# Optimization experiments

Hardware: AMD Instinct MI355X
Metric: run time of the kernel (lower is better)

Reference implementation:

```python
import jax, jax.numpy as jnp
import numpy as np
from jax import lax

B, C, H, W = 8, 48, 256, 256
HEADS = 8
FCT = 16  # self.factor
EPS = 1e-12  # torch F.normalize eps


def setup_inputs() -> dict:
    key = jax.random.key(0)
    k1, k2, k3, k4 = jax.random.split(key, 4)
    x = jax.random.normal(k1, (B, C, H, W), dtype=jnp.float32)
    # qkv 1x1 conv (bias=False): weight (3*dim, dim)
    w_qkv = jax.random.normal(k2, (3 * C, C), dtype=jnp.float32) * 0.05
    # depthwise 3x3 conv, groups = 3*dim: OIHW with I=1
    w_dw = jax.random.normal(k3, (3 * C, 1, 3, 3), dtype=jnp.float32) * 0.05
    # project_out 1x1 conv
    w_proj = jax.random.normal(k4, (C, C), dtype=jnp.float32) * 0.05
    temperature = jnp.ones((HEADS, 1, 1), dtype=jnp.float32)
    return {"x": x, "w_qkv": w_qkv, "w_dw": w_dw, "w_proj": w_proj,
            "temperature": temperature}


def _to_tokens(t):
    # pixel_unshuffle(factor=16) + rearrange
    # 'b (head c fy fx) h w -> b head (fx fy) (c h w)'
    b = t.shape[0]
    c = C // HEADS
    h, w = H // FCT, W // FCT
    # (b, head, c, h, fy, w, fx): pixel_unshuffle channel order is (C, fy, fx)
    t = t.reshape(b, HEADS, c, h, FCT, w, FCT)
    # -> (b, head, fx, fy, c, h, w)
    t = t.transpose(0, 1, 6, 4, 2, 3, 5)
    return t.reshape(b, HEADS, FCT * FCT, c * h * w)


def _from_tokens(t):
    # inverse rearrange + pixel_shuffle(factor=16)
    b = t.shape[0]
    c = C // HEADS
    h, w = H // FCT, W // FCT
    t = t.reshape(b, HEADS, FCT, FCT, c, h, w)  # (b, head, fx, fy, c, h, w)
    # -> (b, head, c, h, fy, w, fx) so final is (b, C, h*FCT, w*FCT)
    t = t.transpose(0, 1, 4, 5, 3, 6, 2)
    return t.reshape(b, C, H, W)


def _l2norm(t):
    n = jnp.sqrt(jnp.sum(t * t, axis=-1, keepdims=True))
    return t / jnp.maximum(n, EPS)


def reference(x, w_qkv, w_dw, w_proj, temperature):
    # H, W are multiples of factor=16 -> pad/unpad are no-ops
    qkv = jnp.einsum('bchw,oc->bohw', x, w_qkv)  # 1x1 conv
    qkv = lax.conv_general_dilated(
        qkv, w_dw, window_strides=(1, 1), padding='SAME',
        feature_group_count=3 * C,
        dimension_numbers=('NCHW', 'OIHW', 'NCHW'))  # depthwise 3x3
    q, k, v = jnp.split(qkv, 3, axis=1)
    q = _l2norm(_to_tokens(q))  # (b, head, 256, c*h*w)
    k = _l2norm(_to_tokens(k))
    v = _to_tokens(v)
    attn = jnp.einsum('bhnd,bhmd->bhnm', q, k) * temperature[None]
    e = jnp.exp(attn)
    attn = e / (jnp.sum(e, axis=-1, keepdims=True) + 1.0)  # softmax_1
    out = jnp.einsum('bhnm,bhmd->bhnd', attn, v)
    out = _from_tokens(out)
    return jnp.einsum('bchw,oc->bohw', out, w_proj)  # project_out
```

## Files before the change

kernel.cpp:

```cpp
#include <hip/hip_runtime.h>
#include <stdint.h>


#define DI __device__ __forceinline__
typedef __attribute__((ext_vector_type(8))) short short8;
typedef __attribute__((ext_vector_type(4))) float f32x4;
typedef __attribute__((ext_vector_type(4))) unsigned short us4;

DI unsigned short f2bf(float f){
  unsigned u = __float_as_uint(f);
  unsigned r = (u + 0x7FFFu + ((u >> 16) & 1u)) >> 16;
  return (unsigned short)r;
}
DI float bf2f(unsigned short h){ return __uint_as_float(((unsigned)h) << 16); }

__global__ __launch_bounds__(256) void k_qkv(const float* __restrict__ x,
                                             const float* __restrict__ wq,
                                             unsigned short* __restrict__ qkv)
{
  __shared__ unsigned short sm[19584];
  unsigned short* const lA = sm;
  unsigned short* const lB = sm + 10368;
  const int t = threadIdx.x;
  const int g0 = blockIdx.x << 7;
  const int b  = g0 >> 16;
  const int p0 = g0 & 65535;

  for (int i = t; i < 9792; i += 256) ((unsigned*)sm)[i] = 0u;
  __syncthreads();
  for (int j = t; j < 6912; j += 256){
    int m = j / 48, k = j - m * 48;
    lA[m * 72 + k] = f2bf(wq[j]);
  }
  for (int j = t; j < 384; j += 256){
    int cp = j >> 4, nc = j & 15;
    const float* xr = x + ((size_t)(b * 48 + 2 * cp)) * 65536 + p0 + nc * 8;
    float4 a0 = *(const float4*)xr;
    float4 a1 = *(const float4*)(xr + 4);
    float4 b0 = *(const float4*)(xr + 65536);
    float4 b1 = *(const float4*)(xr + 65536 + 4);
    float r0[8] = {a0.x,a0.y,a0.z,a0.w,a1.x,a1.y,a1.z,a1.w};
    float r1[8] = {b0.x,b0.y,b0.z,b0.w,b1.x,b1.y,b1.z,b1.w};
    unsigned* dst = (unsigned*)lB;
    int cx = (nc & 7) << 2;
    #pragma unroll
    for (int i = 0; i < 8; i++)
      dst[(nc * 8 + i) * 36 + (cp ^ cx)] =
        (unsigned)f2bf(r0[i]) | ((unsigned)f2bf(r1[i]) << 16);
  }
  __syncthreads();

  const int lane = t & 63, wv = t >> 6;
  const int m15 = lane & 15, quad = lane >> 4;
  const int nw = wv << 5;
  f32x4 acc[9][2];
  f32x4 z = {0.f,0.f,0.f,0.f};
  #pragma unroll
  for (int i = 0; i < 9; i++){ acc[i][0] = z; acc[i][1] = z; }

  #pragma unroll
  for (int ks = 0; ks < 2; ks++){
    short8 bfr[2];
    #pragma unroll
    for (int nt = 0; nt < 2; nt++){
      int row = nw + nt * 16 + m15;
      bfr[nt] = *(const short8*)(lB + row * 72 + (((4 * ks + quad) ^ ((row >> 3) & 7)) << 3));
    }
    #pragma unroll
    for (int mt = 0; mt < 9; mt++){
      short8 afr = *(const short8*)(lA + (mt * 16 + m15) * 72 + ks * 32 + quad * 8);
      acc[mt][0] = __builtin_amdgcn_mfma_f32_16x16x32_bf16(afr, bfr[0], acc[mt][0], 0, 0, 0);
      acc[mt][1] = __builtin_amdgcn_mfma_f32_16x16x32_bf16(afr, bfr[1], acc[mt][1], 0, 0, 0);
    }
  }
  __syncthreads();
  #pragma unroll
  for (int mt = 0; mt < 9; mt++)
    #pragma unroll
    for (int nt = 0; nt < 2; nt++)
      #pragma unroll
      for (int r = 0; r < 4; r++)
        sm[(mt * 16 + quad * 4 + r) * 136 + nw + nt * 16 + m15] = f2bf(acc[mt][nt][r]);
  __syncthreads();
  for (int j = t; j < 2304; j += 256){
    int o = j >> 4, oc = j & 15;
    *(uint4*)(qkv + ((size_t)(b * 144 + o)) * 65536 + p0 + oc * 8) =
      *(const uint4*)(sm + o * 136 + oc * 8);
  }
}

__global__ __launch_bounds__(256, 6) void k_dw(const unsigned short* __restrict__ qkv,
                                               const float* __restrict__ wd,
                                               unsigned short* __restrict__ tok0)
{
  __shared__ unsigned short tile[5184];
  __shared__ unsigned short lout[4224];
  const int t = threadIdx.x;
  const int wg = blockIdx.x, h = blockIdx.y;
  const int b = blockIdx.z / 72, g = blockIdx.z % 72;
  const int ch0 = g * 2;
  const int y0 = h << 4, xg = wg << 7;

  for (int j = t; j < 576; j += 256){
    int rowch = j >> 4, seg = j & 15;
    int cl = rowch >= 18, row = rowch - cl * 18;
    int y = y0 - 1 + row;
    uint4 v = {0u,0u,0u,0u};
    if ((unsigned)y < 256u)
      v = *(const uint4*)(qkv + ((size_t)(b*144 + ch0 + cl))*65536 + y*256 + xg + seg*8);
    *(uint4*)(tile + cl*2592 + row*144 + 8 + seg*8) = v;
  }
  if (t < 72){
    int rowch = t >> 1, side = t & 1;
    int cl = rowch >= 18, row = rowch - cl * 18;
    int y = y0 - 1 + row;
    int xx = side ? (xg + 128) : (xg - 1);
    unsigned short v = 0;
    if ((unsigned)y < 256u && (unsigned)xx < 256u)
      v = qkv[((size_t)(b*144 + ch0 + cl))*65536 + y*256 + xx];
    tile[cl*2592 + row*144 + (side ? 136 : 7)] = v;
  }
  __syncthreads();

  const int xt = t & 31, ys = t >> 5;
  const int x0 = xt << 2;
  #pragma unroll
  for (int cl = 0; cl < 2; cl++){
    int ch = ch0 + cl;
    float w9[9];
    #pragma unroll
    for (int i = 0; i < 9; i++) w9[i] = wd[ch * 9 + i];
    float f[4][6];
    #pragma unroll
    for (int rr = 0; rr < 4; rr++){
      const unsigned short* rp = tile + cl*2592 + (2*ys + rr)*144;
      us4 m = *(const us4*)(rp + 8 + x0);
      unsigned short a = rp[7 + x0];
      unsigned short bb = rp[12 + x0];
      f[rr][0] = bf2f(a);
      f[rr][1] = bf2f(m.x); f[rr][2] = bf2f(m.y);
      f[rr][3] = bf2f(m.z); f[rr][4] = bf2f(m.w);
      f[rr][5] = bf2f(bb);
    }
    #pragma unroll
    for (int r = 0; r < 2; r++)
      #pragma unroll
      for (int k = 0; k < 4; k++){
        float s = 0.f;
        #pragma unroll
        for (int dy = 0; dy < 3; dy++)
          #pragma unroll
          for (int dx = 0; dx < 3; dx++)
            s = fmaf(f[r + dy][k + dx], w9[dy * 3 + dx], s);
        int xl = x0 + k, yo = 2 * ys + r;
        int n = ((xl & 15) << 4) + yo;
        lout[cl*2112 + (xl >> 4)*264 + ((n & 0xF0) | ((n & 15) ^ (n >> 4)))] = f2bf(s);
      }
  }
  __syncthreads();
  for (int j = t; j < 512; j += 256){
    int cl = j >> 8, wt = (j >> 5) & 7, oc = j & 31;
    int split = ch0 / 48;
    int chs = ch0 - split * 48 + cl;
    int head = chs / 6, cc = chs - head * 6;
    int d = cc * 256 + h * 16 + wg * 8 + wt;
    const unsigned short* lp = lout + cl * 2112 + wt * 264;
    unsigned short v8[8];
    #pragma unroll
    for (int i = 0; i < 8; i++){
      int n = oc * 8 + i;
      v8[i] = lp[(n & 0xF0) | ((n & 15) ^ (n >> 4))];
    }
    uint4 pk;
    pk.x = (unsigned)v8[0] | ((unsigned)v8[1] << 16);
    pk.y = (unsigned)v8[2] | ((unsigned)v8[3] << 16);
    pk.z = (unsigned)v8[4] | ((unsigned)v8[5] << 16);
    pk.w = (unsigned)v8[6] | ((unsigned)v8[7] << 16);
    *(uint4*)(tok0 + (size_t)split * 25165824
              + (((size_t)(b * 8 + head)) * 1536 + d) * 256 + oc * 8) = pk;
  }
}

__global__ __launch_bounds__(256) void k_norms(const unsigned short* __restrict__ Qd,
                                               const unsigned short* __restrict__ Kd,
                                               float* __restrict__ nqp,
                                               float* __restrict__ nkp)
{
  const int bh = blockIdx.x, half = blockIdx.z;
  const unsigned short* T = blockIdx.y ? Kd : Qd;
  float* N = blockIdx.y ? nkp : nqp;
  const int t = threadIdx.x, g = t & 7, tl = t >> 3;
  const unsigned short* p = T + (size_t)bh * 393216 + (size_t)(half * 768 + g) * 256 + tl * 8;
  float a[8] = {0.f,0.f,0.f,0.f,0.f,0.f,0.f,0.f};
  #pragma unroll 4
  for (int dd = 0; dd < 96; dd++){
    uint4 v = *(const uint4*)(p + (size_t)dd * 2048);
    const unsigned short* u = (const unsigned short*)&v;
    #pragma unroll
    for (int i = 0; i < 8; i++){ float f = bf2f(u[i]); a[i] = fmaf(f, f, a[i]); }
  }
  #pragma unroll
  for (int off = 1; off < 8; off <<= 1)
    #pragma unroll
    for (int i = 0; i < 8; i++) a[i] += __shfl_xor(a[i], off);
  if (g == 0){
    float* o = N + half * 16384 + bh * 256 + tl * 8;
    #pragma unroll
    for (int i = 0; i < 8; i++) o[i] = a[i];
  }
}

__global__ __launch_bounds__(256) void k_sgemm(const unsigned short* __restrict__ Qd,
                                               const unsigned short* __restrict__ Kd,
                                               float* __restrict__ S)
{
  __shared__ unsigned short sm[18432];
  unsigned short* const sa = sm;
  unsigned short* const sb = sm + 9216;
  const int t = threadIdx.x;
  const int bh = blockIdx.y;
  const int n0 = (blockIdx.x >> 1) << 7;
  const int m0 = (blockIdx.x & 1) << 7;
  const int lane = t & 63, wv = t >> 6;
  const int m15 = lane & 15, quad = lane >> 4;
  const int wm = (wv & 1) << 6, wn = (wv >> 1) << 6;
  const size_t base = (size_t)bh * 393216;
  f32x4 acc[4][4];
  f32x4 z = {0.f,0.f,0.f,0.f};
  #pragma unroll
  for (int i = 0; i < 4; i++)
    #pragma unroll
    for (int j = 0; j < 4; j++) acc[i][j] = z;

  for (int s = 0; s < 24; s++){
    __syncthreads();
    for (int j = t; j < 1024; j += 256){
      int hf = j >> 9, jj = j & 511;
      int kp = jj >> 4, nc = jj & 15;
      const unsigned short* src = (hf ? Kd : Qd) + base
        + (size_t)(s * 64 + 2 * kp) * 256 + (hf ? m0 : n0) + nc * 8;
      uint4 q0 = *(const uint4*)src;
      uint4 q1 = *(const uint4*)(src + 256);
      const unsigned short* u0 = (const unsigned short*)&q0;
      const unsigned short* u1 = (const unsigned short*)&q1;
      unsigned* dst = (unsigned*)(hf ? sb : sa);
      int cx = (nc & 7) << 2;
      #pragma unroll
      for (int i = 0; i < 8; i++)
        dst[(nc * 8 + i) * 36 + (kp ^ cx)] = (unsigned)u0[i] | ((unsigned)u1[i] << 16);
    }
    __syncthreads();
    #pragma unroll
    for (int ks = 0; ks < 2; ks++){
      short8 afr[4], bfr[4];
      #pragma unroll
      for (int i = 0; i < 4; i++){
        int ra = wm + i * 16 + m15;
        int rb = wn + i * 16 + m15;
        afr[i] = *(const short8*)(sa + ra * 72 + (((4 * ks + quad) ^ ((ra >> 3) & 7)) << 3));
        bfr[i] = *(const short8*)(sb + rb * 72 + (((4 * ks + quad) ^ ((rb >> 3) & 7)) << 3));
      }
      #pragma unroll
      for (int mi = 0; mi < 4; mi++)
        #pragma unroll
        for (int ni = 0; ni < 4; ni++)
          acc[mi][ni] = __builtin_amdgcn_mfma_f32_16x16x32_bf16(afr[mi], bfr[ni], acc[mi][ni], 0, 0, 0);
    }
  }
  #pragma unroll
  for (int mi = 0; mi < 4; mi++)
    #pragma unroll
    for (int ni = 0; ni < 4; ni++)
      #pragma unroll
      for (int r = 0; r < 4; r++){
        int nr = n0 + wm + mi * 16 + quad * 4 + r;
        int mc = m0 + wn + ni * 16 + m15;
        S[(size_t)bh * 65536 + (size_t)nr * 256 + mc] = acc[mi][ni][r];
      }
}

__global__ __launch_bounds__(256) void k_softmax(const float* __restrict__ S,
                                                 const float* __restrict__ nqp,
                                                 const float* __restrict__ nkp,
                                                 const float* __restrict__ temp,
                                                 unsigned short* __restrict__ P)
{
  const int t = threadIdx.x, lane = t & 63, wv = t >> 6;
  const int bh = blockIdx.y;
  const int n = blockIdx.x * 4 + wv;
  const float tp = temp[bh & 7];
  const size_t ro = (size_t)bh * 65536 + (size_t)n * 256;
  float4 sv = *(const float4*)(S + ro + lane * 4);
  float4 ka = *(const float4*)(nkp + (size_t)bh * 256 + lane * 4);
  float4 kb = *(const float4*)(nkp + 16384 + (size_t)bh * 256 + lane * 4);
  float nqv = nqp[(size_t)bh * 256 + n] + nqp[16384 + (size_t)bh * 256 + n];
  float qi = tp / fmaxf(sqrtf(fmaxf(nqv, 0.f)), 1e-12f);
  float i0 = 1.f / fmaxf(sqrtf(fmaxf(ka.x + kb.x, 0.f)), 1e-12f);
  float i1 = 1.f / fmaxf(sqrtf(fmaxf(ka.y + kb.y, 0.f)), 1e-12f);
  float i2 = 1.f / fmaxf(sqrtf(fmaxf(ka.z + kb.z, 0.f)), 1e-12f);
  float i3 = 1.f / fmaxf(sqrtf(fmaxf(ka.w + kb.w, 0.f)), 1e-12f);
  float e0 = __expf(fminf(sv.x * qi * i0, 60.f));
  float e1 = __expf(fminf(sv.y * qi * i1, 60.f));
  float e2 = __expf(fminf(sv.z * qi * i2, 60.f));
  float e3 = __expf(fminf(sv.w * qi * i3, 60.f));
  float ss = e0 + e1 + e2 + e3;
  #pragma unroll
  for (int o = 32; o > 0; o >>= 1) ss += __shfl_xor(ss, o);
  float inv = 1.f / (ss + 1.f);
  uint2 pv;
  pv.x = (unsigned)f2bf(e0 * inv) | ((unsigned)f2bf(e1 * inv) << 16);
  pv.y = (unsigned)f2bf(e2 * inv) | ((unsigned)f2bf(e3 * inv) << 16);
  *(uint2*)(P + ro + lane * 4) = pv;
}

__global__ __launch_bounds__(256) void k_ogemm(const unsigned short* __restrict__ Vd,
                                               const unsigned short* __restrict__ P,
                                               unsigned short* __restrict__ Od)
{
  __shared__ unsigned short sm[18432];
  unsigned short* const sa = sm;
  unsigned short* const sb = sm + 9216;
  const int t = threadIdx.x;
  const int bh = blockIdx.y;
  const int d0 = (blockIdx.x >> 1) << 7;
  const int n0 = (blockIdx.x & 1) << 7;
  const int lane = t & 63, wv = t >> 6;
  const int m15 = lane & 15, quad = lane >> 4;
  const int wm = (wv & 1) << 6, wn = (wv >> 1) << 6;
  f32x4 acc[4][4];
  f32x4 z = {0.f,0.f,0.f,0.f};
  #pragma unroll
  for (int i = 0; i < 4; i++)
    #pragma unroll
    for (int j = 0; j < 4; j++) acc[i][j] = z;

  for (int s = 0; s < 4; s++){
    __syncthreads();
    for (int j = t; j < 512; j += 256){
      int hf = j >> 8, jj = j & 255;
      int row = jj >> 1, hh = jj & 1;
      const unsigned short* src = hf
        ? (P  + (size_t)bh * 65536  + (size_t)(n0 + row) * 256 + s * 64 + hh * 32)
        : (Vd + (size_t)bh * 393216 + (size_t)(d0 + row) * 256 + s * 64 + hh * 32);
      uint4 v0 = *(const uint4*)src;
      uint4 v1 = *(const uint4*)(src + 8);
      uint4 v2 = *(const uint4*)(src + 16);
      uint4 v3 = *(const uint4*)(src + 24);
      unsigned* dst = (unsigned*)(hf ? sb : sa) + row * 36 + hh * 16;
      *(uint4*)dst        = v0;
      *(uint4*)(dst + 4)  = v1;
      *(uint4*)(dst + 8)  = v2;
      *(uint4*)(dst + 12) = v3;
    }
    __syncthreads();
    #pragma unroll
    for (int ks = 0; ks < 2; ks++){
      short8 afr[4], bfr[4];
      #pragma unroll
      for (int i = 0; i < 4; i++){
        afr[i] = *(const short8*)(sa + (wm + i * 16 + m15) * 72 + ks * 32 + quad * 8);
        bfr[i] = *(const short8*)(sb + (wn + i * 16 + m15) * 72 + ks * 32 + quad * 8);
      }
      #pragma unroll
      for (int mi = 0; mi < 4; mi++)
        #pragma unroll
        for (int ni = 0; ni < 4; ni++)
          acc[mi][ni] = __builtin_amdgcn_mfma_f32_16x16x32_bf16(afr[mi], bfr[ni], acc[mi][ni], 0, 0, 0);
    }
  }
  __syncthreads();
  #pragma unroll
  for (int mi = 0; mi < 4; mi++)
    #pragma unroll
    for (int ni = 0; ni < 4; ni++)
      #pragma unroll
      for (int r = 0; r < 4; r++)
        sm[(wm + mi * 16 + quad * 4 + r) * 136 + wn + ni * 16 + m15] = f2bf(acc[mi][ni][r]);
  __syncthreads();
  {
    int row = t >> 1, hh = t & 1;
    const unsigned short* lp = sm + row * 136 + hh * 64;
    unsigned short* gp = Od + (size_t)bh * 393216 + (size_t)(d0 + row) * 256 + n0 + hh * 64;
    #pragma unroll
    for (int u = 0; u < 8; u++)
      *(uint4*)(gp + u * 8) = *(const uint4*)(lp + u * 8);
  }
}

__global__ __launch_bounds__(256) void k_proj(const unsigned short* __restrict__ Od,
                                              const float* __restrict__ wp,
                                              float* __restrict__ out)
{
  __shared__ unsigned short sm6[21888];
  unsigned short* const lb = sm6;
  unsigned short* const la = sm6 + 18432;
  float* const lo = (float*)sm6;
  const int t = threadIdx.x;
  const int w = blockIdx.x, h = blockIdx.y, b = blockIdx.z;
  for (int j = t; j < 10944; j += 256) ((unsigned*)sm6)[j] = 0u;
  __syncthreads();
  for (int j = t; j < 2304; j += 256){
    int m = j / 48, k = j - m * 48;
    la[m * 72 + k] = f2bf(wp[j]);
  }
  for (int j = t; j < 768; j += 256){
    int cp = j >> 5, nc = j & 31;
    int ch0 = 2 * cp;
    int head = ch0 / 6, cc = ch0 - head * 6;
    const unsigned short* r0 = Od + (((size_t)(b * 8 + head)) * 1536 + cc * 256 + h * 16 + w) * 256 + nc * 8;
    uint4 q0 = *(const uint4*)r0;
    uint4 q1 = *(const uint4*)(r0 + 65536);
    const unsigned short* u0 = (const unsigned short*)&q0;
    const unsigned short* u1 = (const unsigned short*)&q1;
    unsigned* dst = (unsigned*)lb;
    int cx = (nc & 7) << 2;
    #pragma unroll
    for (int i = 0; i < 8; i++)
      dst[(nc * 8 + i) * 36 + (cp ^ cx)] = (unsigned)u0[i] | ((unsigned)u1[i] << 16);
  }
  __syncthreads();

  const int lane = t & 63, wv = t >> 6;
  const int m15 = lane & 15, quad = lane >> 4;
  const int n0w = wv << 6;
  f32x4 acc[3][4];
  f32x4 z = {0.f,0.f,0.f,0.f};
  #pragma unroll
  for (int i = 0; i < 3; i++)
    #pragma unroll
    for (int j = 0; j < 4; j++) acc[i][j] = z;
  #pragma unroll
  for (int ks = 0; ks < 2; ks++){
    short8 bfr[4];
    #pragma unroll
    for (int nt = 0; nt < 4; nt++){
      int rb = n0w + nt * 16 + m15;
      bfr[nt] = *(const short8*)(lb + rb * 72 + (((4 * ks + quad) ^ ((rb >> 3) & 7)) << 3));
    }
    #pragma unroll
    for (int mt = 0; mt < 3; mt++){
      short8 afr = *(const short8*)(la + (mt * 16 + m15) * 72 + ks * 32 + quad * 8);
      #pragma unroll
      for (int nt = 0; nt < 4; nt++)
        acc[mt][nt] = __builtin_amdgcn_mfma_f32_16x16x32_bf16(afr, bfr[nt], acc[mt][nt], 0, 0, 0);
    }
  }
  for (int mt = 0; mt < 3; mt++){
    __syncthreads();
    #pragma unroll
    for (int nt = 0; nt < 4; nt++)
      #pragma unroll
      for (int r = 0; r < 4; r++){
        int n = n0w + nt * 16 + m15;
        lo[(quad * 4 + r) * 264 + ((n & 0xF0) | ((n & 15) ^ (n >> 4)))] = acc[mt][nt][r];
      }
    __syncthreads();
    int fy = t >> 4, fx = t & 15;
    #pragma unroll
    for (int r = 0; r < 16; r++){
      float v = lo[r * 264 + fx * 16 + (fy ^ fx)];
      out[((size_t)(b * 48 + mt * 16 + r)) * 65536 + (h * 16 + fy) * 256 + w * 16 + fx] = v;
    }
  }
}

extern "C" void kernel_launch(void* const* d_in, const int* in_sizes, int n_in,
                              void* d_out, int out_size, void* d_ws, size_t ws_size,
                              hipStream_t stream)
{
  (void)in_sizes; (void)n_in; (void)out_size; (void)ws_size;
  const float* x  = (const float*)d_in[0];
  const float* wq = (const float*)d_in[1];
  const float* wd = (const float*)d_in[2];
  const float* wp = (const float*)d_in[3];
  const float* tp = (const float*)d_in[4];
  float* out = (float*)d_out;
  char* ws = (char*)d_ws;

  unsigned short* qkv = (unsigned short*)ws;
  unsigned short* Qd  = (unsigned short*)(ws + 150994944);
  unsigned short* Kd  = (unsigned short*)(ws + 201326592);
  unsigned short* Vd  = (unsigned short*)(ws + 251658240);
  float*          S   = (float*)ws;
  unsigned short* P   = (unsigned short*)(ws + 16777216);
  float*          nqp = (float*)(ws + 25165824);
  float*          nkp = (float*)(ws + 25296896);
  unsigned short* Od  = Qd;

  k_qkv    <<<4096,              256, 0, stream>>>(x, wq, qkv);
  k_dw     <<<dim3(2, 16, 576),  256, 0, stream>>>(qkv, wd, Qd);
  k_sgemm  <<<dim3(4, 64),       256, 0, stream>>>(Qd, Kd, S);
  k_norms  <<<dim3(64, 2, 2),    256, 0, stream>>>(Qd, Kd, nqp, nkp);
  k_softmax<<<dim3(64, 64),      256, 0, stream>>>(S, nqp, nkp, tp, P);
  k_ogemm  <<<dim3(24, 64),      256, 0, stream>>>(Vd, P, Od);
  k_proj   <<<dim3(16, 16, 8),   256, 0, stream>>>(Od, wp, out);
}
```

Baseline: 472.7 us.

## Fuse q/k squared-norm reduction into depthwise conv kernel via atomics

Removes the separate k_norms pass, which re-read all of Q and K from memory. The depthwise kernel now accumulates squared outputs per token and adds them into a norm buffer with atomicAdd; k_qkv zeroes that buffer first. The depthwise kernel also switches to a column-major swizzled LDS tile so each thread computes 8 consecutive tokens and writes them straight to global memory, dropping the second LDS staging buffer and a barrier. The cost is atomic traffic, accumulation from bf16-rounded-before-storage values computed in fp32, and a lower occupancy hint.

```diff
diff --git a/kernel.cpp b/kernel.cpp
--- a/kernel.cpp
+++ b/kernel.cpp
@@ -5,7 +5,6 @@
 #define DI __device__ __forceinline__
 typedef __attribute__((ext_vector_type(8))) short short8;
 typedef __attribute__((ext_vector_type(4))) float f32x4;
-typedef __attribute__((ext_vector_type(4))) unsigned short us4;
 
 DI unsigned short f2bf(float f){
   unsigned u = __float_as_uint(f);
@@ -16,7 +15,8 @@
 
 __global__ __launch_bounds__(256) void k_qkv(const float* __restrict__ x,
                                              const float* __restrict__ wq,
-                                             unsigned short* __restrict__ qkv)
+                                             unsigned short* __restrict__ qkv,
+                                             float* __restrict__ nrm)
 {
   __shared__ unsigned short sm[19584];
   unsigned short* const lA = sm;
@@ -25,6 +25,8 @@
   const int g0 = blockIdx.x << 7;
   const int b  = g0 >> 16;
   const int p0 = g0 & 65535;
+
+  if (blockIdx.x < 128) nrm[(blockIdx.x << 8) + t] = 0.f;
 
   for (int i = t; i < 9792; i += 256) ((unsigned*)sm)[i] = 0u;
   __syncthreads();
@@ -89,12 +91,12 @@
   }
 }
 
-__global__ __launch_bounds__(256, 6) void k_dw(const unsigned short* __restrict__ qkv,
+__global__ __launch_bounds__(256, 5) void k_dw(const unsigned short* __restrict__ qkv,
                                                const float* __restrict__ wd,
-                                               unsigned short* __restrict__ tok0)
-{
-  __shared__ unsigned short tile[5184];
-  __shared__ unsigned short lout[4224];
+                                               unsigned short* __restrict__ tok0,
+                                               float* __restrict__ nrm)
+{
+  __shared__ unsigned short tile[8320];
   const int t = threadIdx.x;
   const int wg = blockIdx.x, h = blockIdx.y;
   const int b = blockIdx.z / 72, g = blockIdx.z % 72;
@@ -108,7 +110,15 @@
     uint4 v = {0u,0u,0u,0u};
     if ((unsigned)y < 256u)
       v = *(const uint4*)(qkv + ((size_t)(b*144 + ch0 + cl))*65536 + y*256 + xg + seg*8);
-    *(uint4*)(tile + cl*2592 + row*144 + 8 + seg*8) = v;
+    const unsigned short* u = (const unsigned short*)&v;
+    unsigned short* tb = tile + cl * 4160;
+    int rl = row & 3, rh = row & ~3;
+    #pragma unroll
+    for (int i = 0; i < 8; i++){
+      int ii = (i + seg) & 7;
+      int cx = (seg << 3) + ii + 1;
+      tb[(cx << 5) + ((rh ^ (((cx >> 1) & 7) << 2)) | rl)] = u[ii];
+    }
   }
   if (t < 72){
     int rowch = t >> 1, side = t & 1;
@@ -118,95 +128,74 @@
     unsigned short v = 0;
     if ((unsigned)y < 256u && (unsigned)xx < 256u)
       v = qkv[((size_t)(b*144 + ch0 + cl))*65536 + y*256 + xx];
-    tile[cl*2592 + row*144 + (side ? 136 : 7)] = v;
-  }
-  __syncthreads();
-
-  const int xt = t & 31, ys = t >> 5;
-  const int x0 = xt << 2;
+    int cx = side ? 129 : 0;
+    tile[cl*4160 + (cx << 5) + (((row & ~3) ^ (((cx >> 1) & 7) << 2)) | (row & 3))] = v;
+  }
+  __syncthreads();
+
+  const int xl = t & 127, yg = t >> 7;
+  const int split = ch0 / 48;
+  const int chs = ch0 - split * 48;
+  const int head = chs / 6, ccb = chs - head * 6;
+  const size_t tbase = (size_t)split * 25165824
+                     + ((size_t)(b * 8 + head)) * 393216
+                     + ((size_t)(ccb * 256 + (h << 4) + (wg << 3) + (xl >> 4))) * 256
+                     + ((xl & 15) << 4) + (yg << 3);
+  float acc[8] = {0.f,0.f,0.f,0.f,0.f,0.f,0.f,0.f};
+
   #pragma unroll
   for (int cl = 0; cl < 2; cl++){
-    int ch = ch0 + cl;
     float w9[9];
     #pragma unroll
-    for (int i = 0; i < 9; i++) w9[i] = wd[ch * 9 + i];
-    float f[4][6];
-    #pragma unroll
-    for (int rr = 0; rr < 4; rr++){
-      const unsigned short* rp = tile + cl*2592 + (2*ys + rr)*144;
-      us4 m = *(const us4*)(rp + 8 + x0);
-      unsigned short a = rp[7 + x0];
-      unsigned short bb = rp[12 + x0];
-      f[rr][0] = bf2f(a);
-      f[rr][1] = bf2f(m.x); f[rr][2] = bf2f(m.y);
-      f[rr][3] = bf2f(m.z); f[rr][4] = bf2f(m.w);
-      f[rr][5] = bf2f(bb);
-    }
-    #pragma unroll
-    for (int r = 0; r < 2; r++)
-      #pragma unroll
-      for (int k = 0; k < 4; k++){
-        float s = 0.f;
-        #pragma unroll
-        for (int dy = 0; dy < 3; dy++)
-          #pragma unroll
-          for (int dx = 0; dx < 3; dx++)
-            s = fmaf(f[r + dy][k + dx], w9[dy * 3 + dx], s);
-        int xl = x0 + k, yo = 2 * ys + r;
-        int n = ((xl & 15) << 4) + yo;
-        lout[cl*2112 + (xl >> 4)*264 + ((n & 0xF0) | ((n & 15) ^ (n >> 4)))] = f2bf(s);
-      }
-  }
-  __syncthreads();
-  for (int j = t; j < 512; j += 256){
-    int cl = j >> 8, wt = (j >> 5) & 7, oc = j & 31;
-    int split = ch0 / 48;
-    int chs = ch0 - split * 48 + cl;
-    int head = chs / 6, cc = chs - head * 6;
-    int d = cc * 256 + h * 16 + wg * 8 + wt;
-    const unsigned short* lp = lout + cl * 2112 + wt * 264;
-    unsigned short v8[8];
-    #pragma unroll
-    for (int i = 0; i < 8; i++){
-      int n = oc * 8 + i;
-      v8[i] = lp[(n & 0xF0) | ((n & 15) ^ (n >> 4))];
-    }
+    for (int i = 0; i < 9; i++) w9[i] = wd[(ch0 + cl) * 9 + i];
+    float o[8] = {0.f,0.f,0.f,0.f,0.f,0.f,0.f,0.f};
+    #pragma unroll
+    for (int dx = 0; dx < 3; dx++){
+      int cx = xl + dx;
+      const unsigned short* cb = tile + cl * 4160 + (cx << 5);
+      int swz = ((cx >> 1) & 7) << 2;
+      uint2 va = *(const uint2*)(cb + (((yg << 3)    ) ^ swz));
+      uint2 vb = *(const uint2*)(cb + (((yg << 3) + 4) ^ swz));
+      unsigned vc = *(const unsigned*)(cb + (((yg << 3) + 8) ^ swz));
+      float fv[10];
+      fv[0] = __uint_as_float(va.x << 16);
+      fv[1] = __uint_as_float(va.x & 0xffff0000u);
+      fv[2] = __uint_as_float(va.y << 16);
+      fv[3] = __uint_as_float(va.y & 0xffff0000u);
+      fv[4] = __uint_as_float(vb.x << 16);
+      fv[5] = __uint_as_float(vb.x & 0xffff0000u);
+      fv[6] = __uint_as_float(vb.y << 16);
+      fv[7] = __uint_as_float(vb.y & 0xffff0000u);
+      fv[8] = __uint_as_float(vc << 16);
+      fv[9] = __uint_as_float(vc & 0xffff0000u);
+      #pragma unroll
+      for (int r = 0; r < 8; r++)
+        o[r] = fmaf(fv[r],     w9[dx],
+               fmaf(fv[r + 1], w9[3 + dx],
+               fmaf(fv[r + 2], w9[6 + dx], o[r])));
+    }
+    #pragma unroll
+    for (int r = 0; r < 8; r++) acc[r] = fmaf(o[r], o[r], acc[r]);
     uint4 pk;
-    pk.x = (unsigned)v8[0] | ((unsigned)v8[1] << 16);
-    pk.y = (unsigned)v8[2] | ((unsigned)v8[3] << 16);
-    pk.z = (unsigned)v8[4] | ((unsigned)v8[5] << 16);
-    pk.w = (unsigned)v8[6] | ((unsigned)v8[7] << 16);
-    *(uint4*)(tok0 + (size_t)split * 25165824
-              + (((size_t)(b * 8 + head)) * 1536 + d) * 256 + oc * 8) = pk;
-  }
-}
-
-__global__ __launch_bounds__(256) void k_norms(const unsigned short* __restrict__ Qd,
-                                               const unsigned short* __restrict__ Kd,
-                                               float* __restrict__ nqp,
-                                               float* __restrict__ nkp)
-{
-  const int bh = blockIdx.x, half = blockIdx.z;
-  const unsigned short* T = blockIdx.y ? Kd : Qd;
-  float* N = blockIdx.y ? nkp : nqp;
-  const int t = threadIdx.x, g = t & 7, tl = t >> 3;
-  const unsigned short* p = T + (size_t)bh * 393216 + (size_t)(half * 768 + g) * 256 + tl * 8;
-  float a[8] = {0.f,0.f,0.f,0.f,0.f,0.f,0.f,0.f};
-  #pragma unroll 4
-  for (int dd = 0; dd < 96; dd++){
-    uint4 v = *(const uint4*)(p + (size_t)dd * 2048);
-    const unsigned short* u = (const unsigned short*)&v;
-    #pragma unroll
-    for (int i = 0; i < 8; i++){ float f = bf2f(u[i]); a[i] = fmaf(f, f, a[i]); }
-  }
-  #pragma unroll
-  for (int off = 1; off < 8; off <<= 1)
-    #pragma unroll
-    for (int i = 0; i < 8; i++) a[i] += __shfl_xor(a[i], off);
-  if (g == 0){
-    float* o = N + half * 16384 + bh * 256 + tl * 8;
-    #pragma unroll
-    for (int i = 0; i < 8; i++) o[i] = a[i];
+    asm("v_cvt_pk_bf16_f32 %0, %1, %2" : "=v"(pk.x) : "v"(o[0]), "v"(o[1]));
+    asm("v_cvt_pk_bf16_f32 %0, %1, %2" : "=v"(pk.y) : "v"(o[2]), "v"(o[3]));
+    asm("v_cvt_pk_bf16_f32 %0, %1, %2" : "=v"(pk.z) : "v"(o[4]), "v"(o[5]));
+    asm("v_cvt_pk_bf16_f32 %0, %1, %2" : "=v"(pk.w) : "v"(o[6]), "v"(o[7]));
+    *(uint4*)(tok0 + tbase + (size_t)cl * 65536) = pk;
+  }
+
+  if (split < 2){
+    #pragma unroll
+    for (int r = 0; r < 8; r++){
+      acc[r] += __shfl_xor(acc[r], 16);
+      acc[r] += __shfl_xor(acc[r], 32);
+    }
+    if ((t & 63) < 16){
+      float* dn = nrm + split * 16384 + ((b * 8 + head) << 8)
+                + ((t & 15) << 4) + (yg << 3);
+      #pragma unroll
+      for (int r = 0; r < 8; r++) atomicAdd(dn + r, acc[r]);
+    }
   }
 }
 
@@ -280,8 +269,7 @@
 }
 
 __global__ __launch_bounds__(256) void k_softmax(const float* __restrict__ S,
-                                                 const float* __restrict__ nqp,
-                                                 const float* __restrict__ nkp,
+                                                 const float* __restrict__ nrm,
                                                  const float* __restrict__ temp,
                                                  unsigned short* __restrict__ P)
 {
@@ -291,14 +279,13 @@
   const float tp = temp[bh & 7];
   const size_t ro = (size_t)bh * 65536 + (size_t)n * 256;
   float4 sv = *(const float4*)(S + ro + lane * 4);
-  float4 ka = *(const float4*)(nkp + (size_t)bh * 256 + lane * 4);
-  float4 kb = *(const float4*)(nkp + 16384 + (size_t)bh * 256 + lane * 4);
-  float nqv = nqp[(size_t)bh * 256 + n] + nqp[16384 + (size_t)bh * 256 + n];
+  float4 ka = *(const float4*)(nrm + 16384 + (size_t)bh * 256 + lane * 4);
+  float nqv = nrm[(size_t)bh * 256 + n];
   float qi = tp / fmaxf(sqrtf(fmaxf(nqv, 0.f)), 1e-12f);
-  float i0 = 1.f / fmaxf(sqrtf(fmaxf(ka.x + kb.x, 0.f)), 1e-12f);
-  float i1 = 1.f / fmaxf(sqrtf(fmaxf(ka.y + kb.y, 0.f)), 1e-12f);
-  float i2 = 1.f / fmaxf(sqrtf(fmaxf(ka.z + kb.z, 0.f)), 1e-12f);
-  float i3 = 1.f / fmaxf(sqrtf(fmaxf(ka.w + kb.w, 0.f)), 1e-12f);
+  float i0 = 1.f / fmaxf(sqrtf(fmaxf(ka.x, 0.f)), 1e-12f);
+  float i1 = 1.f / fmaxf(sqrtf(fmaxf(ka.y, 0.f)), 1e-12f);
+  float i2 = 1.f / fmaxf(sqrtf(fmaxf(ka.z, 0.f)), 1e-12f);
+  float i3 = 1.f / fmaxf(sqrtf(fmaxf(ka.w, 0.f)), 1e-12f);
   float e0 = __expf(fminf(sv.x * qi * i0, 60.f));
   float e1 = __expf(fminf(sv.y * qi * i1, 60.f));
   float e2 = __expf(fminf(sv.z * qi * i2, 60.f));
@@ -479,19 +466,17 @@
 
   unsigned short* qkv = (unsigned short*)ws;
   unsigned short* Qd  = (unsigned short*)(ws + 150994944);
-  unsigned short* Kd  = (unsigned short*)(ws + 201326592);
   unsigned short* Vd  = (unsigned short*)(ws + 251658240);
   float*          S   = (float*)ws;
   unsigned short* P   = (unsigned short*)(ws + 16777216);
-  float*          nqp = (float*)(ws + 25165824);
-  float*          nkp = (float*)(ws + 25296896);
+  float*          nrm = (float*)(ws + 301989888);
   unsigned short* Od  = Qd;
-
-  k_qkv    <<<4096,              256, 0, stream>>>(x, wq, qkv);
-  k_dw     <<<dim3(2, 16, 576),  256, 0, stream>>>(qkv, wd, Qd);
+  unsigned short* Kd  = (unsigned short*)(ws + 201326592);
+
+  k_qkv    <<<4096,              256, 0, stream>>>(x, wq, qkv, nrm);
+  k_dw     <<<dim3(2, 16, 576),  256, 0, stream>>>(qkv, wd, Qd, nrm);
   k_sgemm  <<<dim3(4, 64),       256, 0, stream>>>(Qd, Kd, S);
-  k_norms  <<<dim3(64, 2, 2),    256, 0, stream>>>(Qd, Kd, nqp, nkp);
-  k_softmax<<<dim3(64, 64),      256, 0, stream>>>(S, nqp, nkp, tp, P);
+  k_softmax<<<dim3(64, 64),      256, 0, stream>>>(S, nrm, tp, P);
   k_ogemm  <<<dim3(24, 64),      256, 0, stream>>>(Vd, P, Od);
   k_proj   <<<dim3(16, 16, 8),   256, 0, stream>>>(Od, wp, out);
 }
```

After: 1.198 ms. 153% more time.
